# Optimization experiments

Measured on AMD Instinct MI355X. Metric: run time of the kernel, lower is better.

Reference implementation:

```python
import jax, jax.numpy as jnp
import numpy as np

N, HW, CI = 16, 16384, 2
DIM, DEPTH, CO = 256, 4, 3
OMEGA = 30.0
E = CI * DIM + DIM + DEPTH * (DIM * DIM + DIM)  # 263936


def setup_inputs() -> dict:
    key = jax.random.key(0)
    ks = jax.random.split(key, 8)
    x = jax.random.normal(ks[0], (N, HW, CI), jnp.float32)
    weight_offset = jax.random.normal(ks[1], (N, E), jnp.float32) * 0.01
    # layer 0: uniform(-1/ch_in, 1/ch_in); hidden: uniform(-sqrt(6/dim), sqrt(6/dim)); biases zero
    v0 = 1.0 / CI
    w0 = jax.random.uniform(ks[2], (CI, DIM), jnp.float32, -v0, v0)
    b0 = jnp.zeros((DIM,), jnp.float32)
    vh = float(np.sqrt(6.0 / DIM))
    ws_h = jax.random.uniform(ks[3], (DEPTH, DIM, DIM), jnp.float32, -vh, vh)
    bs_h = jnp.zeros((DEPTH, DIM), jnp.float32)
    # output Linear (torch default init bound 1/sqrt(fan_in)); stored as [DIM, CO]
    lim = float(1.0 / np.sqrt(DIM))
    w_out = jax.random.uniform(ks[4], (DIM, CO), jnp.float32, -lim, lim)
    b_out = jax.random.uniform(ks[5], (CO,), jnp.float32, -lim, lim)
    out_scale = jnp.ones((CO,), jnp.float32)  # output_scale coeff = 1.0
    return {"x": x, "weight_offset": weight_offset, "w0": w0, "b0": b0,
            "ws_h": ws_h, "bs_h": bs_h, "w_out": w_out, "b_out": b_out,
            "out_scale": out_scale}


def reference(x, weight_offset, w0, b0, ws_h, bs_h, w_out, b_out, out_scale):
    n = x.shape[0]
    i = CI * DIM
    ow0 = weight_offset[:, :i].reshape(n, CI, DIM)      # [N, CI, DIM]
    ob0 = weight_offset[:, i:i + DIM]                   # [N, DIM]
    i += DIM
    # first layer: per-sample weight = base + offset, then sin(omega * .)
    h = jnp.einsum('nhc,ncd->nhd', x, w0[None] + ow0) + (b0[None] + ob0)[:, None, :]
    h = jnp.sin(OMEGA * h)
    for l in range(DEPTH):
        ow = weight_offset[:, i:i + DIM * DIM].reshape(n, DIM, DIM)
        i += DIM * DIM
        ob = weight_offset[:, i:i + DIM]
        i += DIM
        h = jnp.einsum('nhd,nde->nhe', h, ws_h[l][None] + ow) + (bs_h[l][None] + ob)[:, None, :]
        h = jnp.sin(h)
    return (h @ w_out + b_out) * out_scale
```

## Files before the change

### kernel.cpp

```cpp
#include <hip/hip_runtime.h>


#define N_S 16
#define HW_S 16384
#define E_S 263936
#define INV2PI 0.15915494309189535f
#define OM2PI  4.774648292756860f

typedef _Float16 f16x8 __attribute__((ext_vector_type(8)));
typedef _Float16 f16x4 __attribute__((ext_vector_type(4)));
typedef _Float16 f16x2 __attribute__((ext_vector_type(2)));
typedef float f32x4 __attribute__((ext_vector_type(4)));

#define WT_OFF   0u
#define W0T_OFF  8388608u
#define B0_OFF   8421376u
#define BE_OFF   8437760u

__device__ __forceinline__ float fsin(float z) {
  return __builtin_amdgcn_sinf(__builtin_amdgcn_fractf(z));
}

__global__ __launch_bounds__(256) void siren_pre(
    const float* __restrict__ wo, const float* __restrict__ w0,
    const float* __restrict__ b0, const float* __restrict__ wsh,
    const float* __restrict__ bsh, char* __restrict__ ws)
{
  __shared__ float tile[64][65];
  int b = blockIdx.x, t = threadIdx.x;
  if (b < 1024) {
    int n = b >> 6, rem = b & 63, l = rem >> 4, sub = rem & 15;
    int tk = sub >> 2, te = sub & 3;
    int e_loc = t & 63, ksub = t >> 6;
    const float* wo_n = wo + (size_t)n * E_S + 768 + l * 65792;
    const float* wsh_l = wsh + l * 65536;
    for (int r = 0; r < 16; ++r) {
      int k_loc = ksub * 16 + r;
      int k = tk * 64 + k_loc, e = te * 64 + e_loc;
      tile[k_loc][e_loc] = (wsh_l[k * 256 + e] + wo_n[k * 256 + e]) * INV2PI;
    }
    __syncthreads();
    _Float16* wtl = (_Float16*)(ws + WT_OFF) + (size_t)(n * 4 + l) * 65536;
    int kp = (t & 31) * 2, esub = t >> 5;
    for (int r = 0; r < 8; ++r) {
      int e_loc2 = esub * 8 + r;
      f16x2 hv;
      hv[0] = (_Float16)tile[kp][e_loc2];
      hv[1] = (_Float16)tile[kp + 1][e_loc2];
      int e = te * 64 + e_loc2, k = tk * 64 + kp;
      int c = k >> 5, kin = k & 31;
      *(f16x2*)(wtl + (size_t)c * 8192 + e * 32 + kin) = hv;
    }
  } else if (b == 1024) {
    float* w0t = (float*)(ws + W0T_OFF);
    float* b0e = (float*)(ws + B0_OFF);
    for (int idx = t; idx < 4096; idx += 256) {
      int n = idx >> 8, e = idx & 255;
      const float* wo_n = wo + (size_t)n * E_S;
      float2 v;
      v.x = (w0[e] + wo_n[e]) * OM2PI;
      v.y = (w0[256 + e] + wo_n[256 + e]) * OM2PI;
      *(float2*)(w0t + (n * 256 + e) * 2) = v;
      b0e[n * 256 + e] = (b0[e] + wo_n[512 + e]) * OM2PI;
    }
  } else {
    float* be = (float*)(ws + BE_OFF);
    for (int idx = t; idx < 16384; idx += 256) {
      int n = idx >> 10, rem = idx & 1023, l = rem >> 8, e = rem & 255;
      be[(n * 4 + l) * 256 + e] =
          (bsh[l * 256 + e] + wo[(size_t)n * E_S + 768 + l * 65792 + 65536 + e]) * INV2PI;
    }
  }
}

__global__ __launch_bounds__(512, 2) void siren_main(
    const float* __restrict__ x, const char* __restrict__ ws,
    const float* __restrict__ w_out, const float* __restrict__ b_out,
    const float* __restrict__ out_scale, float* __restrict__ out)
{
  __shared__ __align__(16) unsigned char sH[131072];
  __shared__ __align__(16) unsigned char sW[16384];

  int tid = threadIdx.x;
  int lane = tid & 63, wave = tid >> 6;
  int g = lane >> 4, li = lane & 15;
  int we = wave & 1, wp = wave >> 1;
  int bid = blockIdx.x;
  int n = bid & 15, tile = bid >> 4;

  const char* wt_n = ws + WT_OFF + (size_t)n * 32 * 16384;

  float4 r0, r1;
  {
    const float4* src = (const float4*)wt_n;
    r0 = src[tid];
    r1 = src[tid + 512];
  }

  {
    const float* xp = x + ((size_t)n * HW_S + (size_t)tile * 256) * 2;
    int p = tid & 255;
    float2 xv = *(const float2*)(xp + p * 2);
    const float* w0t = (const float*)(ws + W0T_OFF) + n * 512;
    const float* b0e = (const float*)(ws + B0_OFF) + n * 256;
    int swz = (p & 7) << 4;
    unsigned char* hrow = sH + p * 512;
#pragma unroll
    for (int it = 0; it < 16; ++it) {
      int eg = (tid >> 8) * 16 + it;
      int e0 = eg * 8;
      f32x4 wa = *(const f32x4*)(w0t + e0 * 2);
      f32x4 wb = *(const f32x4*)(w0t + e0 * 2 + 4);
      f32x4 wc = *(const f32x4*)(w0t + e0 * 2 + 8);
      f32x4 wd = *(const f32x4*)(w0t + e0 * 2 + 12);
      f32x4 ba = *(const f32x4*)(b0e + e0);
      f32x4 bb = *(const f32x4*)(b0e + e0 + 4);
      f16x8 hv;
      hv[0] = (_Float16)fsin(fmaf(xv.y, wa[1], fmaf(xv.x, wa[0], ba[0])));
      hv[1] = (_Float16)fsin(fmaf(xv.y, wa[3], fmaf(xv.x, wa[2], ba[1])));
      hv[2] = (_Float16)fsin(fmaf(xv.y, wb[1], fmaf(xv.x, wb[0], ba[2])));
      hv[3] = (_Float16)fsin(fmaf(xv.y, wb[3], fmaf(xv.x, wb[2], ba[3])));
      hv[4] = (_Float16)fsin(fmaf(xv.y, wc[1], fmaf(xv.x, wc[0], bb[0])));
      hv[5] = (_Float16)fsin(fmaf(xv.y, wc[3], fmaf(xv.x, wc[2], bb[1])));
      hv[6] = (_Float16)fsin(fmaf(xv.y, wd[1], fmaf(xv.x, wd[0], bb[2])));
      hv[7] = (_Float16)fsin(fmaf(xv.y, wd[3], fmaf(xv.x, wd[2], bb[3])));
      *(f16x8*)(hrow + ((eg * 16) ^ swz)) = hv;
    }
  }
  {
    int e0 = tid >> 2, sl = tid & 3, e1 = 128 + e0;
    *(float4*)(sW + e0 * 64 + ((sl ^ (e0 & 3)) << 4)) = r0;
    *(float4*)(sW + e1 * 64 + ((sl ^ (e1 & 3)) << 4)) = r1;
  }
  __syncthreads();

  const float* be_n = (const float*)(ws + BE_OFF) + n * 1024;
  f32x4 acc[8][4];

  for (int l = 0; l < 4; ++l) {
    const float* bias = be_n + l * 256;
#pragma unroll
    for (int et = 0; et < 8; ++et) {
      f32x4 bv = *(const f32x4*)(bias + (we * 8 + et) * 16 + g * 4);
#pragma unroll
      for (int pt = 0; pt < 4; ++pt) acc[et][pt] = bv;
    }
    for (int c = 0; c < 8; ++c) {
      int step = l * 8 + c;
      if (step < 31) {
        const float4* src = (const float4*)(wt_n + (size_t)(step + 1) * 16384);
        r0 = src[tid];
        r1 = src[tid + 512];
      }
      f16x8 bfr[4];
#pragma unroll
      for (int pt = 0; pt < 4; ++pt) {
        int p = (wp * 4 + pt) * 16 + li;
        bfr[pt] = *(const f16x8*)(sH + p * 512 + ((c * 64 + g * 16) ^ ((p & 7) << 4)));
      }
#pragma unroll
      for (int et = 0; et < 8; ++et) {
        int e = (we * 8 + et) * 16 + li;
        f16x8 afr = *(const f16x8*)(sW + e * 64 + ((g ^ (li & 3)) << 4));
#pragma unroll
        for (int pt = 0; pt < 4; ++pt)
          acc[et][pt] = __builtin_amdgcn_mfma_f32_16x16x32_f16(afr, bfr[pt], acc[et][pt], 0, 0, 0);
      }
      __syncthreads();
      if (step < 31) {
        int e0 = tid >> 2, sl = tid & 3, e1 = 128 + e0;
        *(float4*)(sW + e0 * 64 + ((sl ^ (e0 & 3)) << 4)) = r0;
        *(float4*)(sW + e1 * 64 + ((sl ^ (e1 & 3)) << 4)) = r1;
      }
      if (c == 7 && l < 3) {
#pragma unroll
        for (int et = 0; et < 8; ++et) {
          int ecol = we * 8 + et;
#pragma unroll
          for (int pt = 0; pt < 4; ++pt) {
            int p = (wp * 4 + pt) * 16 + li;
            f16x4 hv;
#pragma unroll
            for (int r = 0; r < 4; ++r)
              hv[r] = (_Float16)fsin(acc[et][pt][r]);
            *(f16x4*)(sH + p * 512 + ((ecol * 32 + g * 8) ^ ((p & 7) << 4))) = hv;
          }
        }
      }
      __syncthreads();
    }
  }

  float* sWf = (float*)sW;
  for (int i = tid; i < 768; i += 512) sWf[i] = w_out[i];
  __syncthreads();

  float part[4][3];
#pragma unroll
  for (int pt = 0; pt < 4; ++pt)
#pragma unroll
    for (int co = 0; co < 3; ++co) part[pt][co] = 0.f;
#pragma unroll
  for (int et = 0; et < 8; ++et) {
#pragma unroll
    for (int r = 0; r < 4; ++r) {
      int e = (we * 8 + et) * 16 + g * 4 + r;
      float wc0 = sWf[e * 3 + 0], wc1 = sWf[e * 3 + 1], wc2 = sWf[e * 3 + 2];
#pragma unroll
      for (int pt = 0; pt < 4; ++pt) {
        float h = fsin(acc[et][pt][r]);
        part[pt][0] = fmaf(h, wc0, part[pt][0]);
        part[pt][1] = fmaf(h, wc1, part[pt][1]);
        part[pt][2] = fmaf(h, wc2, part[pt][2]);
      }
    }
  }
#pragma unroll
  for (int pt = 0; pt < 4; ++pt)
#pragma unroll
    for (int co = 0; co < 3; ++co) {
      float v = part[pt][co];
      v += __shfl_xor(v, 16);
      v += __shfl_xor(v, 32);
      part[pt][co] = v;
    }
  float* sRed = (float*)sH;
  if (g == 0) {
#pragma unroll
    for (int pt = 0; pt < 4; ++pt) {
      int p = (wp * 4 + pt) * 16 + li;
#pragma unroll
      for (int co = 0; co < 3; ++co)
        sRed[(we * 256 + p) * 3 + co] = part[pt][co];
    }
  }
  __syncthreads();
  float* sFin = (float*)(sH + 8192);
  if (tid < 256) {
    int p = tid;
#pragma unroll
    for (int co = 0; co < 3; ++co)
      sFin[p * 3 + co] =
          (sRed[p * 3 + co] + sRed[(256 + p) * 3 + co] + b_out[co]) * out_scale[co];
  }
  __syncthreads();
  float* op = out + ((size_t)n * HW_S + (size_t)tile * 256) * 3;
  for (int i = tid; i < 768; i += 512) op[i] = sFin[i];
}

extern "C" void kernel_launch(void* const* d_in, const int* in_sizes, int n_in,
                              void* d_out, int out_size, void* d_ws, size_t ws_size,
                              hipStream_t stream) {
  const float* x      = (const float*)d_in[0];
  const float* wo     = (const float*)d_in[1];
  const float* w0     = (const float*)d_in[2];
  const float* b0     = (const float*)d_in[3];
  const float* wsh    = (const float*)d_in[4];
  const float* bsh    = (const float*)d_in[5];
  const float* w_out  = (const float*)d_in[6];
  const float* b_out  = (const float*)d_in[7];
  const float* oscale = (const float*)d_in[8];
  float* out = (float*)d_out;
  char* ws = (char*)d_ws;

  siren_pre<<<1026, 256, 0, stream>>>(wo, w0, b0, wsh, bsh, ws);
  siren_main<<<1024, 512, 0, stream>>>(x, ws, w_out, b_out, oscale, out);
}
```

Before: 185.0 us.

## Load MFMA weight fragments directly from global, halve point tile, drop LDS weight staging

```diff
diff --git a/kernel.cpp b/kernel.cpp
--- a/kernel.cpp
+++ b/kernel.cpp
@@ -73,33 +73,29 @@
   }
 }
 
-__global__ __launch_bounds__(512, 2) void siren_main(
+__global__ __launch_bounds__(256, 2) void siren_main(
     const float* __restrict__ x, const char* __restrict__ ws,
     const float* __restrict__ w_out, const float* __restrict__ b_out,
     const float* __restrict__ out_scale, float* __restrict__ out)
 {
-  __shared__ __align__(16) unsigned char sH[131072];
-  __shared__ __align__(16) unsigned char sW[16384];
+  __shared__ __align__(16) unsigned char sH[65536];
+  __shared__ float sWf[768];
+  __shared__ float sRed[4][128][3];
+  __shared__ float sFin[384];
 
   int tid = threadIdx.x;
-  int lane = tid & 63, wave = tid >> 6;
+  int lane = tid & 63, eq = tid >> 6;
   int g = lane >> 4, li = lane & 15;
-  int we = wave & 1, wp = wave >> 1;
   int bid = blockIdx.x;
   int n = bid & 15, tile = bid >> 4;
 
-  const char* wt_n = ws + WT_OFF + (size_t)n * 32 * 16384;
-
-  float4 r0, r1;
+  const char* wt_n = ws + WT_OFF + (size_t)n * 524288;
+
+  for (int i = tid; i < 768; i += 256) sWf[i] = w_out[i];
+
   {
-    const float4* src = (const float4*)wt_n;
-    r0 = src[tid];
-    r1 = src[tid + 512];
-  }
-
-  {
-    const float* xp = x + ((size_t)n * HW_S + (size_t)tile * 256) * 2;
-    int p = tid & 255;
+    const float* xp = x + ((size_t)n * HW_S + (size_t)tile * 128) * 2;
+    int p = tid & 127;
     float2 xv = *(const float2*)(xp + p * 2);
     const float* w0t = (const float*)(ws + W0T_OFF) + n * 512;
     const float* b0e = (const float*)(ws + B0_OFF) + n * 256;
@@ -107,7 +103,7 @@
     unsigned char* hrow = sH + p * 512;
 #pragma unroll
     for (int it = 0; it < 16; ++it) {
-      int eg = (tid >> 8) * 16 + it;
+      int eg = (tid >> 7) * 16 + it;
       int e0 = eg * 8;
       f32x4 wa = *(const f32x4*)(w0t + e0 * 2);
       f32x4 wb = *(const f32x4*)(w0t + e0 * 2 + 4);
@@ -127,87 +123,70 @@
       *(f16x8*)(hrow + ((eg * 16) ^ swz)) = hv;
     }
   }
-  {
-    int e0 = tid >> 2, sl = tid & 3, e1 = 128 + e0;
-    *(float4*)(sW + e0 * 64 + ((sl ^ (e0 & 3)) << 4)) = r0;
-    *(float4*)(sW + e1 * 64 + ((sl ^ (e1 & 3)) << 4)) = r1;
-  }
   __syncthreads();
 
   const float* be_n = (const float*)(ws + BE_OFF) + n * 1024;
-  f32x4 acc[8][4];
+  int laneoff = (eq * 64 + li) * 64 + g * 16;
+  f32x4 acc[4][8];
 
   for (int l = 0; l < 4; ++l) {
     const float* bias = be_n + l * 256;
 #pragma unroll
-    for (int et = 0; et < 8; ++et) {
-      f32x4 bv = *(const f32x4*)(bias + (we * 8 + et) * 16 + g * 4);
-#pragma unroll
-      for (int pt = 0; pt < 4; ++pt) acc[et][pt] = bv;
-    }
+    for (int et = 0; et < 4; ++et) {
+      f32x4 bv = *(const f32x4*)(bias + eq * 64 + et * 16 + g * 4);
+#pragma unroll
+      for (int pt = 0; pt < 8; ++pt) acc[et][pt] = bv;
+    }
+    const char* wl = wt_n + (size_t)l * 131072 + laneoff;
+#pragma unroll
     for (int c = 0; c < 8; ++c) {
-      int step = l * 8 + c;
-      if (step < 31) {
-        const float4* src = (const float4*)(wt_n + (size_t)(step + 1) * 16384);
-        r0 = src[tid];
-        r1 = src[tid + 512];
-      }
-      f16x8 bfr[4];
-#pragma unroll
-      for (int pt = 0; pt < 4; ++pt) {
-        int p = (wp * 4 + pt) * 16 + li;
+      f16x8 afr[4], bfr[8];
+#pragma unroll
+      for (int et = 0; et < 4; ++et)
+        afr[et] = *(const f16x8*)(wl + c * 16384 + et * 1024);
+#pragma unroll
+      for (int pt = 0; pt < 8; ++pt) {
+        int p = pt * 16 + li;
         bfr[pt] = *(const f16x8*)(sH + p * 512 + ((c * 64 + g * 16) ^ ((p & 7) << 4)));
       }
 #pragma unroll
-      for (int et = 0; et < 8; ++et) {
-        int e = (we * 8 + et) * 16 + li;
-        f16x8 afr = *(const f16x8*)(sW + e * 64 + ((g ^ (li & 3)) << 4));
-#pragma unroll
-        for (int pt = 0; pt < 4; ++pt)
-          acc[et][pt] = __builtin_amdgcn_mfma_f32_16x16x32_f16(afr, bfr[pt], acc[et][pt], 0, 0, 0);
-      }
+      for (int et = 0; et < 4; ++et)
+#pragma unroll
+        for (int pt = 0; pt < 8; ++pt)
+          acc[et][pt] = __builtin_amdgcn_mfma_f32_16x16x32_f16(afr[et], bfr[pt], acc[et][pt], 0, 0, 0);
+    }
+    if (l < 3) {
       __syncthreads();
-      if (step < 31) {
-        int e0 = tid >> 2, sl = tid & 3, e1 = 128 + e0;
-        *(float4*)(sW + e0 * 64 + ((sl ^ (e0 & 3)) << 4)) = r0;
-        *(float4*)(sW + e1 * 64 + ((sl ^ (e1 & 3)) << 4)) = r1;
-      }
-      if (c == 7 && l < 3) {
-#pragma unroll
-        for (int et = 0; et < 8; ++et) {
-          int ecol = we * 8 + et;
-#pragma unroll
-          for (int pt = 0; pt < 4; ++pt) {
-            int p = (wp * 4 + pt) * 16 + li;
-            f16x4 hv;
-#pragma unroll
-            for (int r = 0; r < 4; ++r)
-              hv[r] = (_Float16)fsin(acc[et][pt][r]);
-            *(f16x4*)(sH + p * 512 + ((ecol * 32 + g * 8) ^ ((p & 7) << 4))) = hv;
-          }
+#pragma unroll
+      for (int et = 0; et < 4; ++et) {
+        int eb = eq * 128 + et * 32 + g * 8;
+#pragma unroll
+        for (int pt = 0; pt < 8; ++pt) {
+          int p = pt * 16 + li;
+          f16x4 hv;
+#pragma unroll
+          for (int r = 0; r < 4; ++r)
+            hv[r] = (_Float16)fsin(acc[et][pt][r]);
+          *(f16x4*)(sH + p * 512 + (eb ^ ((p & 7) << 4))) = hv;
         }
       }
       __syncthreads();
     }
   }
 
-  float* sWf = (float*)sW;
-  for (int i = tid; i < 768; i += 512) sWf[i] = w_out[i];
-  __syncthreads();
-
-  float part[4][3];
-#pragma unroll
-  for (int pt = 0; pt < 4; ++pt)
+  float part[8][3];
+#pragma unroll
+  for (int pt = 0; pt < 8; ++pt)
 #pragma unroll
     for (int co = 0; co < 3; ++co) part[pt][co] = 0.f;
 #pragma unroll
-  for (int et = 0; et < 8; ++et) {
+  for (int et = 0; et < 4; ++et) {
 #pragma unroll
     for (int r = 0; r < 4; ++r) {
-      int e = (we * 8 + et) * 16 + g * 4 + r;
+      int e = eq * 64 + et * 16 + g * 4 + r;
       float wc0 = sWf[e * 3 + 0], wc1 = sWf[e * 3 + 1], wc2 = sWf[e * 3 + 2];
 #pragma unroll
-      for (int pt = 0; pt < 4; ++pt) {
+      for (int pt = 0; pt < 8; ++pt) {
         float h = fsin(acc[et][pt][r]);
         part[pt][0] = fmaf(h, wc0, part[pt][0]);
         part[pt][1] = fmaf(h, wc1, part[pt][1]);
@@ -216,7 +195,7 @@
     }
   }
 #pragma unroll
-  for (int pt = 0; pt < 4; ++pt)
+  for (int pt = 0; pt < 8; ++pt)
 #pragma unroll
     for (int co = 0; co < 3; ++co) {
       float v = part[pt][co];
@@ -224,28 +203,27 @@
       v += __shfl_xor(v, 32);
       part[pt][co] = v;
     }
-  float* sRed = (float*)sH;
   if (g == 0) {
 #pragma unroll
-    for (int pt = 0; pt < 4; ++pt) {
-      int p = (wp * 4 + pt) * 16 + li;
+    for (int pt = 0; pt < 8; ++pt) {
+      int p = pt * 16 + li;
 #pragma unroll
       for (int co = 0; co < 3; ++co)
-        sRed[(we * 256 + p) * 3 + co] = part[pt][co];
+        sRed[eq][p][co] = part[pt][co];
     }
   }
   __syncthreads();
-  float* sFin = (float*)(sH + 8192);
-  if (tid < 256) {
+  if (tid < 128) {
     int p = tid;
 #pragma unroll
     for (int co = 0; co < 3; ++co)
-      sFin[p * 3 + co] =
-          (sRed[p * 3 + co] + sRed[(256 + p) * 3 + co] + b_out[co]) * out_scale[co];
+      sFin[p * 3 + co] = (sRed[0][p][co] + sRed[1][p][co] +
+                          sRed[2][p][co] + sRed[3][p][co] +
+                          b_out[co]) * out_scale[co];
   }
   __syncthreads();
-  float* op = out + ((size_t)n * HW_S + (size_t)tile * 256) * 3;
-  for (int i = tid; i < 768; i += 512) op[i] = sFin[i];
+  float* op = out + ((size_t)n * HW_S + (size_t)tile * 128) * 3;
+  for (int i = tid; i < 384; i += 256) op[i] = sFin[i];
 }
 
 extern "C" void kernel_launch(void* const* d_in, const int* in_sizes, int n_in,
@@ -264,5 +242,5 @@
   char* ws = (char*)d_ws;
 
   siren_pre<<<1026, 256, 0, stream>>>(wo, w0, b0, wsh, bsh, ws);
-  siren_main<<<1024, 512, 0, stream>>>(x, ws, w_out, b_out, oscale, out);
-}
+  siren_main<<<2048, 256, 0, stream>>>(x, ws, w_out, b_out, oscale, out);
+}
```

After: 163.1 us. 1.13x faster.
